# Kernel optimization log

Measured on AMD Instinct MI355X. Metric: run time of the kernel, lower is better.

Reference implementation:

```python
import jax, jax.numpy as jnp
import numpy as np

WH, WW = 7, 7
NUM_PRI = 3  # num_priorset=1 -> 3 prior tokens


def _rel_index():
    # Swin relative position index, extended with 3 prior-token columns.
    ch = np.arange(WH)
    cw = np.arange(WW)
    coords = np.stack(np.meshgrid(ch, cw, indexing='ij')).reshape(2, -1)  # [2, N]
    rel = coords[:, :, None] - coords[:, None, :]                          # [2, N, N]
    rel = rel.transpose(1, 2, 0).astype(np.int64)
    rel[..., 0] += WH - 1
    rel[..., 1] += WW - 1
    rel[..., 0] *= 2 * WW - 1
    idx = rel.sum(-1)                                                      # [N, N]
    N = WH * WW
    last = (2 * WH - 1) * (2 * WW - 1)  # 169
    full = np.full((N, N + NUM_PRI), last, dtype=np.int64)
    full[:, :N] = idx
    for j in range(NUM_PRI):
        full[:, N + j] = last + j
    return full

REL_IDX = jnp.asarray(_rel_index())  # [N, N+3]


def setup_inputs() -> dict:
    key = jax.random.key(0)
    ks = jax.random.split(key, 10)
    B, H, W, C = 8, 224, 224, 96
    nW = (H // WH) * (W // WW)  # 1024
    B_ = B * nW                  # 8192
    N = WH * WW                  # 49
    return {
        'x': jax.random.normal(ks[0], (B_, N, C), jnp.float32),
        'mask': jax.random.normal(ks[1], (nW, N, N), jnp.float32),
        'uk_prior': jax.random.normal(ks[2], (B, 1, C), jnp.float32),
        'fg_prior': jax.random.normal(ks[3], (B, 1, C), jnp.float32),
        'bg_prior': jax.random.normal(ks[4], (B, 1, C), jnp.float32),
        'qkv_w': jax.random.normal(ks[5], (3 * C, C), jnp.float32) * 0.02,
        'qkv_b': jax.random.normal(ks[6], (3 * C,), jnp.float32) * 0.02,
        'proj_w': jax.random.normal(ks[7], (C, C), jnp.float32) * 0.02,
        'proj_b': jax.random.normal(ks[8], (C,), jnp.float32) * 0.02,
        'bias_table': jax.random.normal(ks[9], (169 + NUM_PRI, 3), jnp.float32) * 0.02,
        'H': H,
        'W': W,
    }


def reference(x, mask, uk_prior, fg_prior, bg_prior, qkv_w, qkv_b, proj_w, proj_b, bias_table, H, W):
    B_, N, C = x.shape
    nH = bias_table.shape[1]
    hd = C // nH
    scale = hd ** (-0.5)
    nW = (H // WH) * (W // WW)
    B = B_ // nW

    prior_hw = jnp.concatenate([uk_prior, fg_prior, bg_prior], axis=1)  # [B, 3, C]
    # replicate the 3 priors into every window: [B, nW, 3, C] -> [B_, 3, C]
    pri = jnp.broadcast_to(prior_hw[:, None, :, :], (B, nW, NUM_PRI, C)).reshape(B_, NUM_PRI, C)
    x_ext = jnp.concatenate([x, pri], axis=1)                            # [B_, N+3, C]

    qkv = (x_ext @ qkv_w.T + qkv_b).reshape(B_, N + NUM_PRI, 3, nH, hd)
    qkv = qkv.transpose(2, 0, 3, 1, 4)                                   # [3, B_, nH, N+3, hd]
    q, k, v = qkv[0], qkv[1], qkv[2]
    q = q[:, :, :N, :] * scale                                           # [B_, nH, N, hd]

    attn = jnp.einsum('bhnd,bhmd->bhnm', q, k)                           # [B_, nH, N, N+3]
    bias = bias_table[REL_IDX]                                           # [N, N+3, nH]
    attn = attn + bias.transpose(2, 0, 1)[None]

    mask_p = jnp.pad(mask, ((0, 0), (0, 0), (0, NUM_PRI)))               # [nW, N, N+3]
    attn = attn.reshape(B, nW, nH, N, N + NUM_PRI) + mask_p[None, :, None]
    attn = jax.nn.softmax(attn.reshape(B_, nH, N, N + NUM_PRI), axis=-1)

    out = jnp.einsum('bhnm,bhmd->bnhd', attn, v).reshape(B_, N, C)
    out = out @ proj_w.T + proj_b

    # prior highway: run qkv on the raw priors, take v, project
    qkv_hw = (prior_hw @ qkv_w.T + qkv_b).reshape(B, NUM_PRI, 3, nH, hd)
    v_hw = qkv_hw[:, :, 2].reshape(B, NUM_PRI, C)
    v_hw = v_hw @ proj_w.T + proj_b
    return out, v_hw
```

## Files before the change

### kernel.cpp

```cpp
#include <hip/hip_runtime.h>
#include <hip/hip_bf16.h>


typedef __bf16 bf16x8 __attribute__((ext_vector_type(8)));
typedef float  f32x4  __attribute__((ext_vector_type(4)));
typedef short  s16x4  __attribute__((ext_vector_type(4)));
typedef unsigned short u16x4 __attribute__((ext_vector_type(4)));
using bf16 = __hip_bfloat16;

#define SCALE 0.17677669529663687f

#define LDS_XQ    0
#define LDS_K     4900
#define LDS_P     10100
#define LDS_VT    13432
#define LDS_TOT   19960

static __device__ inline float s2f(unsigned short s) {
    unsigned int u = ((unsigned int)s) << 16;
    float f;
    __builtin_memcpy(&f, &u, 4);
    return f;
}
static __device__ inline short f2s(float f) {
    __bf16 h = (__bf16)f;
    short s;
    __builtin_memcpy(&s, &h, 2);
    return s;
}
static __device__ inline bf16x8 ldw8(const float* p) {
    f32x4 a = *reinterpret_cast<const f32x4*>(p);
    f32x4 b = *reinterpret_cast<const f32x4*>(p + 4);
    bf16x8 r;
    #pragma unroll
    for (int i = 0; i < 4; ++i) {
        r[i]     = (__bf16)a[i];
        r[i + 4] = (__bf16)b[i];
    }
    return r;
}

__global__ __launch_bounds__(256)
void pawsa_prep(const float* __restrict__ qkv_w, const float* __restrict__ proj_w,
                const float* __restrict__ bias_table, bf16* __restrict__ ws)
{
    int blk = blockIdx.x, t = threadIdx.x;
    if (blk < 144) {
        int i = blk * 256 + t;
        if (i < 27648)      ws[i] = __float2bfloat16(qkv_w[i]);
        else if (i < 36864) ws[i] = __float2bfloat16(proj_w[i - 27648]);
        return;
    }
    int lane = t & 63, wid = t >> 6;
    int lr = lane & 15, lg = lane >> 4;
    u16x4* bg = reinterpret_cast<u16x4*>(ws + 36864);
    for (int h = 0; h < 3; ++h) {
        for (int nt = 0; nt < 4; ++nt) {
            int c = nt * 16 + lr;
            u16x4 v4;
            for (int j = 0; j < 4; ++j) {
                int n = wid * 16 + lg * 4 + j;
                int idx = 171;
                if (c < 49) {
                    idx = (n / 7 - c / 7 + 6) * 13 + ((n % 7) - (c % 7) + 6);
                    if (idx > 171 || idx < 0) idx = 171;
                } else if (c < 52) {
                    idx = 169 + (c - 49);
                }
                short s = f2s(bias_table[idx * 3 + h]);
                v4[j] = (unsigned short)s;
            }
            bg[(h * 4 + nt) * 256 + t] = v4;
        }
    }
}

__global__ __launch_bounds__(256, 4)
void pawsa_main(const float* __restrict__ x, const float* __restrict__ mask,
                const float* __restrict__ uk, const float* __restrict__ fg,
                const float* __restrict__ bg,
                const bf16* __restrict__ wq,
                const float* __restrict__ qkv_b,
                const bf16* __restrict__ wp,
                const float* __restrict__ proj_b,
                const u16x4* __restrict__ biasg,
                float* __restrict__ out)
{
    __shared__ short smem[LDS_TOT];

    const int tid  = threadIdx.x;
    const int w    = blockIdx.x;
    const int b    = w >> 10;
    const int wi   = w & 1023;
    const int lane = tid & 63;
    const int wid  = tid >> 6;
    const int lr   = lane & 15;
    const int lg   = lane >> 4;

    bf16x8 af[3][4];
    #pragma unroll
    for (int mt = 0; mt < 4; ++mt) {
        int n = mt * 16 + lr;
        #pragma unroll
        for (int ks = 0; ks < 3; ++ks) {
            bf16x8 a = (bf16x8)0;
            if (n < 49) {
                a = ldw8(x + ((size_t)w * 49 + n) * 96 + ks * 32 + lg * 8);
            } else if (n < 52) {
                const float* pr = (n == 49) ? uk : (n == 50) ? fg : bg;
                a = ldw8(pr + b * 96 + ks * 32 + lg * 8);
            }
            af[ks][mt] = a;
        }
    }

    const int nt0 = (wid < 3) ? wid * 5 : 13;
    #pragma unroll
    for (int i = 0; i < 5; ++i) {
        int o = (nt0 + i) * 16 + lr;
        bf16x8 bw0 = *reinterpret_cast<const bf16x8*>(wq + o * 96 +  0 + lg * 8);
        bf16x8 bw1 = *reinterpret_cast<const bf16x8*>(wq + o * 96 + 32 + lg * 8);
        bf16x8 bw2 = *reinterpret_cast<const bf16x8*>(wq + o * 96 + 64 + lg * 8);
        float  qb  = qkv_b[o];
        f32x4 acc[4] = {(f32x4)0.f, (f32x4)0.f, (f32x4)0.f, (f32x4)0.f};
        #pragma unroll
        for (int mt = 0; mt < 4; ++mt) {
            acc[mt] = __builtin_amdgcn_mfma_f32_16x16x32_bf16(af[0][mt], bw0, acc[mt], 0, 0, 0);
            acc[mt] = __builtin_amdgcn_mfma_f32_16x16x32_bf16(af[1][mt], bw1, acc[mt], 0, 0, 0);
            acc[mt] = __builtin_amdgcn_mfma_f32_16x16x32_bf16(af[2][mt], bw2, acc[mt], 0, 0, 0);
        }
        int s = o / 96;
        int rem = o - s * 96;
        #pragma unroll
        for (int mt = 0; mt < 4; ++mt) {
            if (s == 2) {
                s16x4 pk;
                #pragma unroll
                for (int j = 0; j < 4; ++j) pk[j] = f2s(acc[mt][j] + qb);
                *reinterpret_cast<s16x4*>(
                    &smem[LDS_VT + rem * 68 + mt * 16 + lg * 4]) = pk;
            } else {
                #pragma unroll
                for (int j = 0; j < 4; ++j) {
                    int n = mt * 16 + lg * 4 + j;
                    short hv = f2s(acc[mt][j] + qb);
                    if (s == 0) { if (n < 49) smem[LDS_XQ + n * 100 + rem] = hv; }
                    else        { if (n < 52) smem[LDS_K  + n * 100 + rem] = hv; }
                }
            }
        }
    }

    float mk[4][4];
    #pragma unroll
    for (int nt = 0; nt < 4; ++nt) {
        int c = nt * 16 + lr;
        #pragma unroll
        for (int j = 0; j < 4; ++j) {
            int n = wid * 16 + lg * 4 + j;
            float m = 0.f;
            if (c < 49 && n < 49)
                m = mask[(size_t)wi * 2401 + n * 49 + c];
            mk[nt][j] = m;
        }
    }
    u16x4 bgv[12];
    #pragma unroll
    for (int i = 0; i < 12; ++i) bgv[i] = biasg[i * 256 + tid];

    __syncthreads();

    #pragma unroll
    for (int h = 0; h < 3; ++h) {
        bf16x8 aq = *reinterpret_cast<const bf16x8*>(
            &smem[LDS_XQ + (wid * 16 + lr) * 100 + h * 32 + lg * 8]);
        f32x4 sacc[4];
        #pragma unroll
        for (int nt = 0; nt < 4; ++nt) {
            bf16x8 bk = *reinterpret_cast<const bf16x8*>(
                &smem[LDS_K + (nt * 16 + lr) * 100 + h * 32 + lg * 8]);
            sacc[nt] = __builtin_amdgcn_mfma_f32_16x16x32_bf16(aq, bk, (f32x4)0.f, 0, 0, 0);
        }
        float lgt[4][4];
        #pragma unroll
        for (int nt = 0; nt < 4; ++nt) {
            int c = nt * 16 + lr;
            u16x4 bgq = bgv[h * 4 + nt];
            #pragma unroll
            for (int j = 0; j < 4; ++j) {
                float v = -1e30f;
                if (c < 52)
                    v = sacc[nt][j] * SCALE + s2f(bgq[j]) + mk[nt][j];
                lgt[nt][j] = v;
            }
        }
        float pr[4][4];
        #pragma unroll
        for (int j = 0; j < 4; ++j) {
            float m = fmaxf(fmaxf(lgt[0][j], lgt[1][j]), fmaxf(lgt[2][j], lgt[3][j]));
            m = fmaxf(m, __shfl_xor(m, 1));
            m = fmaxf(m, __shfl_xor(m, 2));
            m = fmaxf(m, __shfl_xor(m, 4));
            m = fmaxf(m, __shfl_xor(m, 8));
            float sum = 0.f;
            #pragma unroll
            for (int nt = 0; nt < 4; ++nt) {
                pr[nt][j] = __expf(lgt[nt][j] - m);
                sum += pr[nt][j];
            }
            sum += __shfl_xor(sum, 1);
            sum += __shfl_xor(sum, 2);
            sum += __shfl_xor(sum, 4);
            sum += __shfl_xor(sum, 8);
            float inv = 1.0f / sum;
            #pragma unroll
            for (int nt = 0; nt < 4; ++nt) pr[nt][j] *= inv;
        }
        #pragma unroll
        for (int nt = 0; nt < 4; ++nt)
            #pragma unroll
            for (int j = 0; j < 4; ++j) {
                int prow = wid * 16 + lg * 4 + j;
                if (prow < 49)
                    smem[LDS_P + prow * 68 + nt * 16 + lr] = f2s(pr[nt][j]);
            }

        f32x4 ov[2] = {(f32x4)0.f, (f32x4)0.f};
        #pragma unroll
        for (int ks = 0; ks < 2; ++ks) {
            bf16x8 ap = *reinterpret_cast<const bf16x8*>(
                &smem[LDS_P + (wid * 16 + lr) * 68 + ks * 32 + lg * 8]);
            #pragma unroll
            for (int nt2 = 0; nt2 < 2; ++nt2) {
                bf16x8 bv = *reinterpret_cast<const bf16x8*>(
                    &smem[LDS_VT + (h * 32 + nt2 * 16 + lr) * 68 + ks * 32 + lg * 8]);
                ov[nt2] = __builtin_amdgcn_mfma_f32_16x16x32_bf16(ap, bv, ov[nt2], 0, 0, 0);
            }
        }
        #pragma unroll
        for (int nt2 = 0; nt2 < 2; ++nt2)
            #pragma unroll
            for (int j = 0; j < 4; ++j) {
                int orow = wid * 16 + lg * 4 + j;
                if (orow < 49)
                    smem[LDS_XQ + orow * 100 + h * 32 + nt2 * 16 + lr]
                        = f2s(ov[nt2][j]);
            }
    }

    f32x4 po[6];
    #pragma unroll
    for (int nt = 0; nt < 6; ++nt) po[nt] = (f32x4)0.f;
    #pragma unroll
    for (int ks = 0; ks < 3; ++ks) {
        bf16x8 a = *reinterpret_cast<const bf16x8*>(
            &smem[LDS_XQ + (wid * 16 + lr) * 100 + ks * 32 + lg * 8]);
        #pragma unroll
        for (int nt = 0; nt < 6; ++nt) {
            bf16x8 bp = *reinterpret_cast<const bf16x8*>(
                wp + (nt * 16 + lr) * 96 + ks * 32 + lg * 8);
            po[nt] = __builtin_amdgcn_mfma_f32_16x16x32_bf16(a, bp, po[nt], 0, 0, 0);
        }
    }
    #pragma unroll
    for (int nt = 0; nt < 6; ++nt) {
        float pb = proj_b[nt * 16 + lr];
        #pragma unroll
        for (int j = 0; j < 4; ++j) {
            int n = wid * 16 + lg * 4 + j;
            if (n < 49)
                out[((size_t)w * 49 + n) * 96 + nt * 16 + lr] = po[nt][j] + pb;
        }
    }
}

__global__ __launch_bounds__(128)
void pawsa_prior(const float* __restrict__ uk, const float* __restrict__ fg,
                 const float* __restrict__ bg,
                 const float* __restrict__ qkv_w, const float* __restrict__ qkv_b,
                 const float* __restrict__ proj_w, const float* __restrict__ proj_b,
                 float* __restrict__ out_vhw)
{
    int blk = blockIdx.x;
    int b = blk / 3, p = blk % 3;
    int t = threadIdx.x;
    __shared__ float prr[96], vf[96];
    const float* src = (p == 0) ? uk : (p == 1) ? fg : bg;
    if (t < 96) prr[t] = src[b * 96 + t];
    __syncthreads();
    if (t < 96) {
        float acc = qkv_b[192 + t];
        for (int k = 0; k < 96; ++k)
            acc += prr[k] * qkv_w[(192 + t) * 96 + k];
        vf[t] = acc;
    }
    __syncthreads();
    if (t < 96) {
        float acc = proj_b[t];
        for (int c = 0; c < 96; ++c)
            acc += vf[c] * proj_w[t * 96 + c];
        out_vhw[(b * 3 + p) * 96 + t] = acc;
    }
}

extern "C" void kernel_launch(void* const* d_in, const int* in_sizes, int n_in,
                              void* d_out, int out_size, void* d_ws, size_t ws_size,
                              hipStream_t stream) {
    const float* x          = (const float*)d_in[0];
    const float* mask       = (const float*)d_in[1];
    const float* uk         = (const float*)d_in[2];
    const float* fg         = (const float*)d_in[3];
    const float* bg         = (const float*)d_in[4];
    const float* qkv_w      = (const float*)d_in[5];
    const float* qkv_b      = (const float*)d_in[6];
    const float* proj_w     = (const float*)d_in[7];
    const float* proj_b     = (const float*)d_in[8];
    const float* bias_table = (const float*)d_in[9];
    float* out = (float*)d_out;
    bf16* ws   = (bf16*)d_ws;

    pawsa_prep<<<145, 256, 0, stream>>>(qkv_w, proj_w, bias_table, ws);
    pawsa_prior<<<24, 128, 0, stream>>>(uk, fg, bg, qkv_w, qkv_b, proj_w, proj_b,
                                        out + (size_t)8192 * 49 * 96);
    pawsa_main<<<8192, 256, 0, stream>>>(x, mask, uk, fg, bg,
                                         ws, qkv_b, ws + 27648, proj_b,
                                         (const u16x4*)(ws + 36864), out);
}
```

Baseline: 239.7 us.

## Transpose attention MFMAs and keep P and O in registers via bpermute

Swaps the operand order of the QK^T and PV MFMAs so each lane owns one query row. Softmax now reduces with two cross-group shuffles instead of four. The probabilities and attention outputs are packed to bf16 and redistributed into MFMA A-fragments with ds_bpermute, no longer written to and read back from LDS. This removes the P buffer, shrinks the LDS footprint and loads bias per head instead of holding all of it in registers, at the cost of extra permute instructions and more accumulator registers.

```diff
diff --git a/kernel.cpp b/kernel.cpp
--- a/kernel.cpp
+++ b/kernel.cpp
@@ -6,15 +6,15 @@
 typedef float  f32x4  __attribute__((ext_vector_type(4)));
 typedef short  s16x4  __attribute__((ext_vector_type(4)));
 typedef unsigned short u16x4 __attribute__((ext_vector_type(4)));
+typedef int    i32x4  __attribute__((ext_vector_type(4)));
 using bf16 = __hip_bfloat16;
 
 #define SCALE 0.17677669529663687f
 
 #define LDS_XQ    0
-#define LDS_K     4900
-#define LDS_P     10100
-#define LDS_VT    13432
-#define LDS_TOT   19960
+#define LDS_K     4802
+#define LDS_VT    10002
+#define LDS_TOT   16338
 
 static __device__ inline float s2f(unsigned short s) {
     unsigned int u = ((unsigned int)s) << 16;
@@ -28,6 +28,11 @@
     __builtin_memcpy(&s, &h, 2);
     return s;
 }
+static __device__ inline int pk2(float a, float b) {
+    unsigned int lo = (unsigned short)f2s(a);
+    unsigned int hi = (unsigned short)f2s(b);
+    return (int)(lo | (hi << 16));
+}
 static __device__ inline bf16x8 ldw8(const float* p) {
     f32x4 a = *reinterpret_cast<const f32x4*>(p);
     f32x4 b = *reinterpret_cast<const f32x4*>(p + 4);
@@ -38,6 +43,23 @@
         r[i + 4] = (__bf16)b[i];
     }
     return r;
+}
+static __device__ inline bf16x8 xfrag(int c00, int c01, int c10, int c11,
+                                      int iA, int iB, int selHi) {
+    int a0 = __builtin_amdgcn_ds_bpermute(iA, c00);
+    int a1 = __builtin_amdgcn_ds_bpermute(iA, c10);
+    int h0 = __builtin_amdgcn_ds_bpermute(iA, c01);
+    int h1 = __builtin_amdgcn_ds_bpermute(iA, c11);
+    int b0 = __builtin_amdgcn_ds_bpermute(iB, c00);
+    int b1 = __builtin_amdgcn_ds_bpermute(iB, c10);
+    int g0 = __builtin_amdgcn_ds_bpermute(iB, c01);
+    int g1 = __builtin_amdgcn_ds_bpermute(iB, c11);
+    i32x4 r;
+    r[0] = selHi ? a1 : a0;
+    r[1] = selHi ? h1 : h0;
+    r[2] = selHi ? b1 : b0;
+    r[3] = selHi ? g1 : g0;
+    return __builtin_bit_cast(bf16x8, r);
 }
 
 __global__ __launch_bounds__(256)
@@ -53,22 +75,21 @@
     }
     int lane = t & 63, wid = t >> 6;
     int lr = lane & 15, lg = lane >> 4;
+    int q = wid * 16 + lr;
     u16x4* bg = reinterpret_cast<u16x4*>(ws + 36864);
     for (int h = 0; h < 3; ++h) {
         for (int nt = 0; nt < 4; ++nt) {
-            int c = nt * 16 + lr;
             u16x4 v4;
             for (int j = 0; j < 4; ++j) {
-                int n = wid * 16 + lg * 4 + j;
+                int key = nt * 16 + lg * 4 + j;
                 int idx = 171;
-                if (c < 49) {
-                    idx = (n / 7 - c / 7 + 6) * 13 + ((n % 7) - (c % 7) + 6);
-                    if (idx > 171 || idx < 0) idx = 171;
-                } else if (c < 52) {
-                    idx = 169 + (c - 49);
+                if (key < 49) {
+                    if (q < 49)
+                        idx = (q / 7 - key / 7 + 6) * 13 + (q % 7 - key % 7 + 6);
+                } else if (key < 52) {
+                    idx = 169 + (key - 49);
                 }
-                short s = f2s(bias_table[idx * 3 + h]);
-                v4[j] = (unsigned short)s;
+                v4[j] = (unsigned short)f2s(bias_table[idx * 3 + h]);
             }
             bg[(h * 4 + nt) * 256 + t] = v4;
         }
@@ -96,6 +117,11 @@
     const int wid  = tid >> 6;
     const int lr   = lane & 15;
     const int lg   = lane >> 4;
+    const int q    = wid * 16 + lr;
+
+    const int iA = (lr + ((lg & 1) << 5)) << 2;
+    const int iB = (lr + ((lg & 1) << 5) + 16) << 2;
+    const int selHi = (lg >= 2);
 
     bf16x8 af[3][4];
     #pragma unroll
@@ -138,13 +164,13 @@
                 #pragma unroll
                 for (int j = 0; j < 4; ++j) pk[j] = f2s(acc[mt][j] + qb);
                 *reinterpret_cast<s16x4*>(
-                    &smem[LDS_VT + rem * 68 + mt * 16 + lg * 4]) = pk;
+                    &smem[LDS_VT + rem * 66 + mt * 16 + lg * 4]) = pk;
             } else {
                 #pragma unroll
                 for (int j = 0; j < 4; ++j) {
                     int n = mt * 16 + lg * 4 + j;
                     short hv = f2s(acc[mt][j] + qb);
-                    if (s == 0) { if (n < 49) smem[LDS_XQ + n * 100 + rem] = hv; }
+                    if (s == 0) { if (n < 49) smem[LDS_XQ + n * 98  + rem] = hv; }
                     else        { if (n < 52) smem[LDS_K  + n * 100 + rem] = hv; }
                 }
             }
@@ -154,112 +180,110 @@
     float mk[4][4];
     #pragma unroll
     for (int nt = 0; nt < 4; ++nt) {
-        int c = nt * 16 + lr;
         #pragma unroll
         for (int j = 0; j < 4; ++j) {
-            int n = wid * 16 + lg * 4 + j;
+            int key = nt * 16 + lg * 4 + j;
             float m = 0.f;
-            if (c < 49 && n < 49)
-                m = mask[(size_t)wi * 2401 + n * 49 + c];
+            if (q < 49 && key < 49)
+                m = mask[(size_t)wi * 2401 + q * 49 + key];
             mk[nt][j] = m;
         }
     }
-    u16x4 bgv[12];
-    #pragma unroll
-    for (int i = 0; i < 12; ++i) bgv[i] = biasg[i * 256 + tid];
 
     __syncthreads();
 
+    f32x4 oacc[6];
+    #pragma unroll
+    for (int T = 0; T < 6; ++T) oacc[T] = (f32x4)0.f;
+
     #pragma unroll
     for (int h = 0; h < 3; ++h) {
+        u16x4 bgq[4];
+        #pragma unroll
+        for (int nt = 0; nt < 4; ++nt) bgq[nt] = biasg[(h * 4 + nt) * 256 + tid];
+
         bf16x8 aq = *reinterpret_cast<const bf16x8*>(
-            &smem[LDS_XQ + (wid * 16 + lr) * 100 + h * 32 + lg * 8]);
+            &smem[LDS_XQ + q * 98 + h * 32 + lg * 8]);
         f32x4 sacc[4];
         #pragma unroll
         for (int nt = 0; nt < 4; ++nt) {
             bf16x8 bk = *reinterpret_cast<const bf16x8*>(
                 &smem[LDS_K + (nt * 16 + lr) * 100 + h * 32 + lg * 8]);
-            sacc[nt] = __builtin_amdgcn_mfma_f32_16x16x32_bf16(aq, bk, (f32x4)0.f, 0, 0, 0);
+            sacc[nt] = __builtin_amdgcn_mfma_f32_16x16x32_bf16(bk, aq, (f32x4)0.f, 0, 0, 0);
         }
         float lgt[4][4];
         #pragma unroll
         for (int nt = 0; nt < 4; ++nt) {
-            int c = nt * 16 + lr;
-            u16x4 bgq = bgv[h * 4 + nt];
             #pragma unroll
             for (int j = 0; j < 4; ++j) {
+                int key = nt * 16 + lg * 4 + j;
                 float v = -1e30f;
-                if (c < 52)
-                    v = sacc[nt][j] * SCALE + s2f(bgq[j]) + mk[nt][j];
+                if (key < 52)
+                    v = sacc[nt][j] * SCALE + s2f(bgq[nt][j]) + mk[nt][j];
                 lgt[nt][j] = v;
             }
         }
-        float pr[4][4];
-        #pragma unroll
-        for (int j = 0; j < 4; ++j) {
-            float m = fmaxf(fmaxf(lgt[0][j], lgt[1][j]), fmaxf(lgt[2][j], lgt[3][j]));
-            m = fmaxf(m, __shfl_xor(m, 1));
-            m = fmaxf(m, __shfl_xor(m, 2));
-            m = fmaxf(m, __shfl_xor(m, 4));
-            m = fmaxf(m, __shfl_xor(m, 8));
-            float sum = 0.f;
-            #pragma unroll
-            for (int nt = 0; nt < 4; ++nt) {
-                pr[nt][j] = __expf(lgt[nt][j] - m);
-                sum += pr[nt][j];
-            }
-            sum += __shfl_xor(sum, 1);
-            sum += __shfl_xor(sum, 2);
-            sum += __shfl_xor(sum, 4);
-            sum += __shfl_xor(sum, 8);
-            float inv = 1.0f / sum;
-            #pragma unroll
-            for (int nt = 0; nt < 4; ++nt) pr[nt][j] *= inv;
-        }
+        float m = lgt[0][0];
         #pragma unroll
         for (int nt = 0; nt < 4; ++nt)
             #pragma unroll
+            for (int j = 0; j < 4; ++j) m = fmaxf(m, lgt[nt][j]);
+        m = fmaxf(m, __shfl_xor(m, 16));
+        m = fmaxf(m, __shfl_xor(m, 32));
+        float p[4][4], sum = 0.f;
+        #pragma unroll
+        for (int nt = 0; nt < 4; ++nt)
+            #pragma unroll
             for (int j = 0; j < 4; ++j) {
-                int prow = wid * 16 + lg * 4 + j;
-                if (prow < 49)
-                    smem[LDS_P + prow * 68 + nt * 16 + lr] = f2s(pr[nt][j]);
-            }
-
-        f32x4 ov[2] = {(f32x4)0.f, (f32x4)0.f};
+                p[nt][j] = __expf(lgt[nt][j] - m);
+                sum += p[nt][j];
+            }
+        sum += __shfl_xor(sum, 16);
+        sum += __shfl_xor(sum, 32);
+        float inv = 1.0f / sum;
+        #pragma unroll
+        for (int nt = 0; nt < 4; ++nt)
+            #pragma unroll
+            for (int j = 0; j < 4; ++j) p[nt][j] *= inv;
+
+        int pd[4][2];
+        #pragma unroll
+        for (int nt = 0; nt < 4; ++nt) {
+            pd[nt][0] = pk2(p[nt][0], p[nt][1]);
+            pd[nt][1] = pk2(p[nt][2], p[nt][3]);
+        }
         #pragma unroll
         for (int ks = 0; ks < 2; ++ks) {
-            bf16x8 ap = *reinterpret_cast<const bf16x8*>(
-                &smem[LDS_P + (wid * 16 + lr) * 68 + ks * 32 + lg * 8]);
-            #pragma unroll
-            for (int nt2 = 0; nt2 < 2; ++nt2) {
-                bf16x8 bv = *reinterpret_cast<const bf16x8*>(
-                    &smem[LDS_VT + (h * 32 + nt2 * 16 + lr) * 68 + ks * 32 + lg * 8]);
-                ov[nt2] = __builtin_amdgcn_mfma_f32_16x16x32_bf16(ap, bv, ov[nt2], 0, 0, 0);
-            }
-        }
-        #pragma unroll
-        for (int nt2 = 0; nt2 < 2; ++nt2)
-            #pragma unroll
-            for (int j = 0; j < 4; ++j) {
-                int orow = wid * 16 + lg * 4 + j;
-                if (orow < 49)
-                    smem[LDS_XQ + orow * 100 + h * 32 + nt2 * 16 + lr]
-                        = f2s(ov[nt2][j]);
-            }
-    }
-
+            bf16x8 pf = xfrag(pd[2 * ks][0], pd[2 * ks][1],
+                              pd[2 * ks + 1][0], pd[2 * ks + 1][1], iA, iB, selHi);
+            #pragma unroll
+            for (int a = 0; a < 2; ++a) {
+                bf16x8 vt = *reinterpret_cast<const bf16x8*>(
+                    &smem[LDS_VT + (h * 32 + a * 16 + lr) * 66 + ks * 32 + lg * 8]);
+                oacc[h * 2 + a] = __builtin_amdgcn_mfma_f32_16x16x32_bf16(
+                    vt, pf, oacc[h * 2 + a], 0, 0, 0);
+            }
+        }
+    }
+
+    int od[6][2];
+    #pragma unroll
+    for (int T = 0; T < 6; ++T) {
+        od[T][0] = pk2(oacc[T][0], oacc[T][1]);
+        od[T][1] = pk2(oacc[T][2], oacc[T][3]);
+    }
     f32x4 po[6];
     #pragma unroll
     for (int nt = 0; nt < 6; ++nt) po[nt] = (f32x4)0.f;
     #pragma unroll
     for (int ks = 0; ks < 3; ++ks) {
-        bf16x8 a = *reinterpret_cast<const bf16x8*>(
-            &smem[LDS_XQ + (wid * 16 + lr) * 100 + ks * 32 + lg * 8]);
+        bf16x8 of = xfrag(od[2 * ks][0], od[2 * ks][1],
+                          od[2 * ks + 1][0], od[2 * ks + 1][1], iA, iB, selHi);
         #pragma unroll
         for (int nt = 0; nt < 6; ++nt) {
             bf16x8 bp = *reinterpret_cast<const bf16x8*>(
                 wp + (nt * 16 + lr) * 96 + ks * 32 + lg * 8);
-            po[nt] = __builtin_amdgcn_mfma_f32_16x16x32_bf16(a, bp, po[nt], 0, 0, 0);
+            po[nt] = __builtin_amdgcn_mfma_f32_16x16x32_bf16(of, bp, po[nt], 0, 0, 0);
         }
     }
     #pragma unroll
```

Measured after the change: 241.3 us. About the same (+0.7%).
